# Optimization experiments

Measured on AMD Instinct MI355X. Metric: run time of the kernel, lower is better.

## Reference

```python
import jax, jax.numpy as jnp
import numpy as np

NEG = -9e15
ALPHA = 0.2  # LeakyReLU slope


def xavier(key, shape, gain=1.414):
    fan_in, fan_out = shape[-2], shape[-1]
    bound = gain * np.sqrt(6.0 / (fan_in + fan_out))
    return jax.random.uniform(key, shape, jnp.float32, -bound, bound)


def setup_inputs() -> dict:
    key = jax.random.key(0)
    ks = jax.random.split(key, 8)
    N, D_IN, HID, OUT, H = 4096, 128, 64, 64, 4
    x = jax.random.normal(ks[0], (N, D_IN), jnp.float32)
    adj = jax.random.randint(ks[1], (N, N), 0, 2, jnp.int32)
    # layer 0: in=D_IN, out=HID, heads=H
    W0 = xavier(ks[2], (H, D_IN, HID))
    a0 = xavier(ks[3], (H, 2 * HID, 1))
    # layer 1: in=HID*H, out=HID, heads=H
    W1 = xavier(ks[4], (H, HID * H, HID))
    a1 = xavier(ks[5], (H, 2 * HID, 1))
    # layer 2: in=HID*H, out=OUT, heads=1
    W2 = xavier(ks[6], (1, HID * H, OUT))
    a2 = xavier(ks[7], (1, 2 * OUT, 1))
    return {"x": x, "adj": adj, "W0": W0, "a0": a0, "W1": W1, "a1": a1, "W2": W2, "a2": a2}


def gat_layer(x, adj_mask, W, a):
    # x: [N, D], W: [H, D, O], a: [H, 2O, 1]
    O = W.shape[-1]
    h = jnp.einsum('nd,hdo->hno', x, W)                      # [H, N, O]
    a_l, a_r = a[:, :O, 0], a[:, O:, 0]                      # [H, O] each
    e_l = jnp.einsum('hno,ho->hn', h, a_l)                   # a^T[Wh_i||Wh_j] split
    e_r = jnp.einsum('hno,ho->hn', h, a_r)
    e = e_l[:, :, None] + e_r[:, None, :]                    # [H, N, N]
    e = jnp.where(e > 0, e, ALPHA * e)                       # LeakyReLU
    att = jnp.where(adj_mask[None], e, NEG)
    att = jax.nn.softmax(att, axis=-1)                       # dropout skipped (eval)
    out = jnp.einsum('hnm,hmo->hno', att, h)                 # [H, N, O]
    N = x.shape[0]
    return out.transpose(1, 0, 2).reshape(N, -1)             # [N, H*O]


def reference(x, adj, W0, a0, W1, a1, W2, a2):
    adj_mask = adj > 0
    h = gat_layer(x, adj_mask, W0, a0)
    h = jax.nn.elu(h)
    h = gat_layer(h, adj_mask, W1, a1)
    h = jax.nn.elu(h)
    h = gat_layer(h, adj_mask, W2, a2)
    return h
```

## Files before the change

### kernel.cpp

```cpp
#include <hip/hip_runtime.h>

#define LOG2E 1.4426950408889634f

typedef float  f32x4 __attribute__((ext_vector_type(4)));
typedef int    i32x4 __attribute__((ext_vector_type(4)));
typedef short  s16x8 __attribute__((ext_vector_type(8)));
typedef unsigned long long u64x2 __attribute__((ext_vector_type(2)));

static __device__ __forceinline__ float exp2_fast(float x) {
#if __has_builtin(__builtin_amdgcn_exp2f)
    return __builtin_amdgcn_exp2f(x);
#else
    return exp2f(x);
#endif
}
static __device__ __forceinline__ unsigned short bf16_rne(float f) {
    unsigned u = __float_as_uint(f);
    u += 0x7FFFu + ((u >> 16) & 1u);
    return (unsigned short)(u >> 16);
}
static __device__ __forceinline__ int sbfe1(unsigned w, int pos) {
#if __has_builtin(__builtin_amdgcn_sbfe)
    return __builtin_amdgcn_sbfe((int)w, pos, 1);
#else
    return (int)(w << (31 - pos)) >> 31;
#endif
}
static __device__ __forceinline__ unsigned pack_hi16(unsigned u1, unsigned u0) {
#if __has_builtin(__builtin_amdgcn_perm)
    return __builtin_amdgcn_perm(u1, u0, 0x07060302u);
#else
    return (u0 >> 16) | (u1 & 0xFFFF0000u);
#endif
}

__global__ __launch_bounds__(256) void prep_all(
    const float* __restrict__ xf, const int* __restrict__ adj,
    const float* __restrict__ W0, const float* __restrict__ W1,
    const float* __restrict__ W2,
    unsigned short* __restrict__ xc, unsigned long long* __restrict__ bits,
    unsigned short* __restrict__ W0t, unsigned short* __restrict__ W1t,
    unsigned short* __restrict__ W2t, unsigned* __restrict__ MxU)
{
    const int b = blockIdx.x, tid = threadIdx.x;
    if (b < 16384) {
        const int w = tid >> 6, lane = tid & 63;
        const int base = b * 1024 + w * 256;
        unsigned long long m[4];
#pragma unroll
        for (int r = 0; r < 4; ++r)
            m[r] = __ballot(adj[base + r * 64 + lane] != 0);
        if (lane == 0) {
            u64x2 lo = {m[0], m[1]}, hi = {m[2], m[3]};
            *(u64x2*)(bits + (base >> 6))     = lo;
            *(u64x2*)(bits + (base >> 6) + 2) = hi;
        }
    } else if (b < 18432) {
        int i = (b - 16384) * 256 + tid;
        xc[i] = bf16_rne(xf[i]);
    } else {
        int gid = (b - 18432) * 256 + tid;
        if (gid < 32768) {
            int h = gid >> 13, d = (gid >> 6) & 127, o = gid & 63;
            W0t[(h * 64 + o) * 128 + d] = bf16_rne(W0[gid]);
        } else if (gid < 98304) {
            int g = gid - 32768;
            int h = g >> 14, d = (g >> 6) & 255, o = g & 63;
            W1t[(h * 64 + o) * 256 + d] = bf16_rne(W1[g]);
        } else if (gid < 114688) {
            int g = gid - 98304;
            int d = g >> 6, o = g & 63;
            W2t[o * 256 + d] = bf16_rne(W2[g]);
        } else if (gid < 114700) {
            MxU[gid - 114688] = 0x007FFFFFu;
        }
    }
}

__global__ __launch_bounds__(256) void gemm_elr(
    const unsigned short* __restrict__ X, int K,
    const unsigned short* __restrict__ Wt,
    const float* __restrict__ a,
    unsigned short* __restrict__ hT,
    float* __restrict__ el2, float* __restrict__ er2,
    unsigned* __restrict__ MxU)
{
    const int lane = threadIdx.x & 63, w = threadIdx.x >> 6;
    const int c = lane & 15, q = lane >> 4;
    const int h = blockIdx.y;
    const int nb = blockIdx.x * 64 + w * 16;
    const unsigned short* xrow = X + (size_t)(nb + c) * K + q * 8;
    const unsigned short* wb   = Wt + ((size_t)h * 64 + c) * K + q * 8;

    f32x4 acc[4] = {{0,0,0,0},{0,0,0,0},{0,0,0,0},{0,0,0,0}};
    for (int kk = 0; kk < K; kk += 32) {
        s16x8 af = *(const s16x8*)(xrow + kk);
#pragma unroll
        for (int j = 0; j < 4; ++j) {
            s16x8 bf = *(const s16x8*)(wb + (size_t)(j * 16) * K + kk);
            acc[j] = __builtin_amdgcn_mfma_f32_16x16x32_bf16(af, bf, acc[j], 0, 0, 0);
        }
    }
#pragma unroll
    for (int j = 0; j < 4; ++j) {
        unsigned d0 = (unsigned)bf16_rne(acc[j][0]) | ((unsigned)bf16_rne(acc[j][1]) << 16);
        unsigned d1 = (unsigned)bf16_rne(acc[j][2]) | ((unsigned)bf16_rne(acc[j][3]) << 16);
        unsigned short* dst = hT + ((size_t)h * 64 + j * 16 + c) * 4096 + nb + q * 4;
        ((unsigned*)dst)[0] = d0;
        ((unsigned*)dst)[1] = d1;
    }
    const float* ab = a + h * 128;
    float elr[4] = {0,0,0,0}, err[4] = {0,0,0,0};
#pragma unroll
    for (int j = 0; j < 4; ++j) {
        float al = ab[j * 16 + c];
        float ar = ab[64 + j * 16 + c];
#pragma unroll
        for (int r = 0; r < 4; ++r) {
            elr[r] = fmaf(al, acc[j][r], elr[r]);
            err[r] = fmaf(ar, acc[j][r], err[r]);
        }
    }
#pragma unroll
    for (int m = 1; m <= 8; m <<= 1) {
#pragma unroll
        for (int r = 0; r < 4; ++r) {
            elr[r] += __shfl_xor(elr[r], m, 64);
            err[r] += __shfl_xor(err[r], m, 64);
        }
    }
    if (c == 0) {
#pragma unroll
        for (int r = 0; r < 4; ++r) {
            int n = nb + q * 4 + r;
            el2[h * 4096 + n] = elr[r] * LOG2E;
            er2[h * 4096 + n] = err[r] * LOG2E;
        }
    }
    float mm = fmaxf(fmaxf(err[0], err[1]), fmaxf(err[2], err[3]));
    mm = fmaxf(mm, __shfl_xor(mm, 16, 64));
    mm = fmaxf(mm, __shfl_xor(mm, 32, 64));
    if (lane == 0) {
        unsigned u = __float_as_uint(mm * LOG2E);
        unsigned key = (u & 0x80000000u) ? ~u : (u | 0x80000000u);
        atomicMax(MxU + h, key);
    }
}

__global__ __launch_bounds__(256) void att_kernel(
    const unsigned short* __restrict__ hT,
    const float* __restrict__ el2g, const float* __restrict__ er2g,
    const unsigned* __restrict__ MxU,
    const unsigned long long* __restrict__ bits,
    float* __restrict__ accP, float* __restrict__ lP,
    int H, int KPS, int HO)
{
    __shared__ unsigned short ldsH[64 * 256];
    __shared__ float ldsE[512];
    const int tid = threadIdx.x;
    const int lane = tid & 63, w = tid >> 6;
    const int c = lane & 15, q = lane >> 4, q8 = q * 8;
    const int h = blockIdx.y, ks = blockIdx.z;
    const int nb = blockIdx.x * 64 + w * 16;
    const int rowA = nb + c;

    unsigned kM = MxU[h];
    float M2 = __uint_as_float((kM & 0x80000000u) ? (kM & 0x7FFFFFFFu) : ~kM);
    float e2 = el2g[h * 4096 + rowA];
    float xx = e2 + M2;
    float C2 = fmaxf(xx, 0.2f * xx);
    const float Al = exp2_fast(xx - C2);
    const float Bl = exp2_fast(fmaf(0.2f, xx, -C2));

    const char* bitrow = (const char*)bits + (size_t)rowA * 512 + (size_t)(KPS >> 3) * ks;

    s16x8 ones = {0,0,0,0,0,0,0,0};
    if (c == 0) {
#pragma unroll
        for (int i = 0; i < 8; ++i) ones[i] = (short)0x3F80;
    }
    f32x4 acc[4] = {{0,0,0,0},{0,0,0,0},{0,0,0,0},{0,0,0,0}};
    f32x4 accl = {0,0,0,0};

    const unsigned short* hTh = hT + (size_t)h * 64 * 4096;
    const float* erh = er2g + h * 4096;
    const int tiles = KPS >> 8;

    for (int t = 0; t < tiles; ++t) {
        const int mabs = ks * KPS + t * 256;
#pragma unroll
        for (int i = 0; i < 8; ++i) {
            int cidx = i * 256 + tid;
            int o = cidx >> 5, seg = cidx & 31;
            i32x4 v = *(const i32x4*)(hTh + (size_t)o * 4096 + mabs + seg * 8);
            *(i32x4*)(ldsH + o * 256 + ((seg ^ (o & 7)) << 3)) = v;
        }
        {
            float er = erh[mabs + tid] - M2;
            ldsE[2 * tid]     = exp2_fast(er);
            ldsE[2 * tid + 1] = exp2_fast(0.2f * er);
        }
        __syncthreads();

        i32x4 b0 = *(const i32x4*)(bitrow + t * 32);
        i32x4 b1 = *(const i32x4*)(bitrow + t * 32 + 16);
        int bw[8] = {b0[0], b0[1], b0[2], b0[3], b1[0], b1[1], b1[2], b1[3]};

#pragma unroll
        for (int cc = 0; cc < 8; ++cc) {
            const int kl = cc * 32 + q8;
            const f32x4* ep = (const f32x4*)(ldsE + 2 * kl);
            f32x4 ev0 = ep[0], ev1 = ep[1], ev2 = ep[2], ev3 = ep[3];
            const unsigned word = (unsigned)bw[cc];
            unsigned pd[4];
#pragma unroll
            for (int jj = 0; jj < 4; ++jj) {
                f32x4 ev = (jj == 0) ? ev0 : (jj == 1) ? ev1 : (jj == 2) ? ev2 : ev3;
                float p0 = fmaxf(Al * ev[0], Bl * ev[1]);
                float p1 = fmaxf(Al * ev[2], Bl * ev[3]);
                unsigned u0 = __float_as_uint(p0) & (unsigned)sbfe1(word, q8 + 2 * jj);
                unsigned u1 = __float_as_uint(p1) & (unsigned)sbfe1(word, q8 + 2 * jj + 1);
                pd[jj] = pack_hi16(u1, u0);
            }
            union { unsigned u[4]; s16x8 s; } afu;
            afu.u[0] = pd[0]; afu.u[1] = pd[1]; afu.u[2] = pd[2]; afu.u[3] = pd[3];
            s16x8 af = afu.s;
            const int klx = kl ^ ((c & 7) << 3);
            const unsigned short* lb = ldsH + c * 256 + klx;
#pragma unroll
            for (int j = 0; j < 4; ++j) {
                s16x8 bf = *(const s16x8*)(lb + (size_t)(j * 16) * 256);
                acc[j] = __builtin_amdgcn_mfma_f32_16x16x32_bf16(af, bf, acc[j], 0, 0, 0);
            }
            accl = __builtin_amdgcn_mfma_f32_16x16x32_bf16(af, ones, accl, 0, 0, 0);
        }
        __syncthreads();
    }
    float ls[4];
#pragma unroll
    for (int r = 0; r < 4; ++r) ls[r] = __shfl(accl[r], lane & 48, 64);

    float* ap = accP + ((size_t)ks * 4096 + nb + q * 4) * HO + h * 64 + c;
#pragma unroll
    for (int r = 0; r < 4; ++r)
#pragma unroll
        for (int j = 0; j < 4; ++j)
            ap[(size_t)r * HO + j * 16] = acc[j][r];
    if (c == 0) {
#pragma unroll
        for (int r = 0; r < 4; ++r)
            lP[((size_t)ks * H + h) * 4096 + nb + q * 4 + r] = ls[r];
    }
}

__global__ __launch_bounds__(256) void comb_kernel(
    const float* __restrict__ accP, const float* __restrict__ lP,
    unsigned short* __restrict__ outb, float* __restrict__ outf,
    int KS, int H, int lgHO, int do_elu)
{
    const int idx = blockIdx.x * 256 + threadIdx.x;
    const int HO = 1 << lgHO;
    const int n = idx >> lgHO, col = idx & (HO - 1), h = col >> 6;
    float s = 0.f, l = 0.f;
    for (int ks = 0; ks < KS; ++ks) {
        s += accP[((size_t)ks * 4096 + n) * HO + col];
        l += lP[((size_t)ks * H + h) * 4096 + n];
    }
    float v = s / l;
    if (do_elu && v < 0.f) v = exp2_fast(v * LOG2E) - 1.f;
    if (outf) outf[idx] = v;
    else      outb[idx] = bf16_rne(v);
}

extern "C" void kernel_launch(void* const* d_in, const int* in_sizes, int n_in,
                              void* d_out, int out_size, void* d_ws, size_t ws_size,
                              hipStream_t stream)
{
    (void)in_sizes; (void)n_in; (void)out_size; (void)ws_size;
    const float* x   = (const float*)d_in[0];
    const int*   adj = (const int*)d_in[1];
    const float* W0  = (const float*)d_in[2];
    const float* a0  = (const float*)d_in[3];
    const float* W1  = (const float*)d_in[4];
    const float* a1  = (const float*)d_in[5];
    const float* W2  = (const float*)d_in[6];
    const float* a2  = (const float*)d_in[7];

    char* p = (char*)d_ws;
    unsigned long long* bits = (unsigned long long*)(p + 0x000000);
    unsigned short* hT  = (unsigned short*)(p + 0x200000);
    unsigned short* X12 = (unsigned short*)(p + 0x400000);
    unsigned short* Xc  = (unsigned short*)(p + 0x600000);
    unsigned short* W0t = (unsigned short*)(p + 0x700000);
    unsigned short* W1t = (unsigned short*)(p + 0x710000);
    unsigned short* W2t = (unsigned short*)(p + 0x730000);
    float*    el2  = (float*)(p + 0x738000);
    float*    er2  = (float*)(p + 0x748000);
    unsigned* MxU  = (unsigned*)(p + 0x758000);
    float*    accP = (float*)(p + 0x760000);
    float*    lP   = (float*)(p + 0xF60000);

    prep_all<<<18881, 256, 0, stream>>>(x, adj, W0, W1, W2, Xc, bits,
                                        W0t, W1t, W2t, MxU);

    gemm_elr<<<dim3(64, 4), 256, 0, stream>>>(Xc, 128, W0t, a0, hT, el2, er2, MxU + 0);
    att_kernel<<<dim3(64, 4, 2), 256, 0, stream>>>(hT, el2, er2, MxU + 0, bits, accP, lP, 4, 2048, 256);
    comb_kernel<<<4096, 256, 0, stream>>>(accP, lP, X12, nullptr, 2, 4, 8, 1);

    gemm_elr<<<dim3(64, 4), 256, 0, stream>>>(X12, 256, W1t, a1, hT, el2, er2, MxU + 4);
    att_kernel<<<dim3(64, 4, 2), 256, 0, stream>>>(hT, el2, er2, MxU + 4, bits, accP, lP, 4, 2048, 256);
    comb_kernel<<<4096, 256, 0, stream>>>(accP, lP, X12, nullptr, 2, 4, 8, 1);

    gemm_elr<<<dim3(64, 1), 256, 0, stream>>>(X12, 256, W2t, a2, hT, el2, er2, MxU + 8);
    att_kernel<<<dim3(64, 1, 4), 256, 0, stream>>>(hT, el2, er2, MxU + 8, bits, accP, lP, 1, 1024, 64);
    comb_kernel<<<1024, 256, 0, stream>>>(accP, lP, nullptr, (float*)d_out, 4, 1, 6, 0);
}
```

Measured before the change: 276.6 us.

## Double-buffer attention tiles with direct global-to-LDS loads and prefetch

```diff
diff --git a/kernel.cpp b/kernel.cpp
--- a/kernel.cpp
+++ b/kernel.cpp
@@ -155,8 +155,8 @@
     float* __restrict__ accP, float* __restrict__ lP,
     int H, int KPS, int HO)
 {
-    __shared__ unsigned short ldsH[64 * 256];
-    __shared__ float ldsE[512];
+    __shared__ unsigned short ldsH[2][64 * 256];
+    __shared__ float ldsE[2][512];
     const int tid = threadIdx.x;
     const int lane = tid & 63, w = tid >> 6;
     const int c = lane & 15, q = lane >> 4, q8 = q * 8;
@@ -173,44 +173,72 @@
     const float Bl = exp2_fast(fmaf(0.2f, xx, -C2));
 
     const char* bitrow = (const char*)bits + (size_t)rowA * 512 + (size_t)(KPS >> 3) * ks;
-
-    s16x8 ones = {0,0,0,0,0,0,0,0};
-    if (c == 0) {
-#pragma unroll
-        for (int i = 0; i < 8; ++i) ones[i] = (short)0x3F80;
-    }
-    f32x4 acc[4] = {{0,0,0,0},{0,0,0,0},{0,0,0,0},{0,0,0,0}};
-    f32x4 accl = {0,0,0,0};
-
     const unsigned short* hTh = hT + (size_t)h * 64 * 4096;
     const float* erh = er2g + h * 4096;
     const int tiles = KPS >> 8;
-
-    for (int t = 0; t < tiles; ++t) {
-        const int mabs = ks * KPS + t * 256;
+    const int kbase = ks * KPS;
+
+    auto STAGE = [&](int buf, int mabs_) {
 #pragma unroll
         for (int i = 0; i < 8; ++i) {
             int cidx = i * 256 + tid;
-            int o = cidx >> 5, seg = cidx & 31;
-            i32x4 v = *(const i32x4*)(hTh + (size_t)o * 4096 + mabs + seg * 8);
-            *(i32x4*)(ldsH + o * 256 + ((seg ^ (o & 7)) << 3)) = v;
-        }
-        {
-            float er = erh[mabs + tid] - M2;
-            ldsE[2 * tid]     = exp2_fast(er);
-            ldsE[2 * tid + 1] = exp2_fast(0.2f * er);
-        }
-        __syncthreads();
-
-        i32x4 b0 = *(const i32x4*)(bitrow + t * 32);
-        i32x4 b1 = *(const i32x4*)(bitrow + t * 32 + 16);
-        int bw[8] = {b0[0], b0[1], b0[2], b0[3], b1[0], b1[1], b1[2], b1[3]};
+            int o = cidx >> 5, g = cidx & 31;
+            const unsigned short* sp =
+                hTh + (size_t)o * 4096 + mabs_ + ((g ^ (o & 7)) << 3);
+            unsigned short* dp = &ldsH[buf][(i * 256 + (tid & ~63)) << 3];
+            __builtin_amdgcn_global_load_lds(
+                (const __attribute__((address_space(1))) void*)sp,
+                (__attribute__((address_space(3))) void*)dp, 16, 0, 0);
+        }
+    };
+
+    s16x8 ones = {0,0,0,0,0,0,0,0};
+    if (c == 0) {
+#pragma unroll
+        for (int i = 0; i < 8; ++i) ones[i] = (short)0x3F80;
+    }
+    f32x4 acc[4] = {{0,0,0,0},{0,0,0,0},{0,0,0,0},{0,0,0,0}};
+    f32x4 accl = {0,0,0,0};
+
+    STAGE(0, kbase);
+    {
+        float ee = erh[kbase + tid] - M2;
+        ldsE[0][2 * tid]     = exp2_fast(ee);
+        ldsE[0][2 * tid + 1] = exp2_fast(0.2f * ee);
+    }
+    i32x4 bA = *(const i32x4*)(bitrow);
+    i32x4 bB = *(const i32x4*)(bitrow + 16);
+    __syncthreads();
+
+    for (int t = 0; t < tiles; ++t) {
+        const int cur = t & 1, nxt = cur ^ 1;
+        const bool more = (t + 1 < tiles);
+        const unsigned short* Hc = ldsH[cur];
+        const float* Ec = ldsE[cur];
+
+        const f32x4* ep0 = (const f32x4*)(Ec + 2 * q8);
+        f32x4 nv0 = ep0[0], nv1 = ep0[1], nv2 = ep0[2], nv3 = ep0[3];
+
+        float ern = 0.f;
+        if (more) {
+            const int mn = kbase + (t + 1) * 256;
+            STAGE(nxt, mn);
+            ern = erh[mn + tid];
+        }
+        int bw[8] = {bA[0], bA[1], bA[2], bA[3], bB[0], bB[1], bB[2], bB[3]};
+        if (more) {
+            bA = *(const i32x4*)(bitrow + (t + 1) * 32);
+            bB = *(const i32x4*)(bitrow + (t + 1) * 32 + 16);
+        }
 
 #pragma unroll
         for (int cc = 0; cc < 8; ++cc) {
+            f32x4 ev0 = nv0, ev1 = nv1, ev2 = nv2, ev3 = nv3;
+            if (cc < 7) {
+                const f32x4* epn = (const f32x4*)(Ec + 2 * ((cc + 1) * 32 + q8));
+                nv0 = epn[0]; nv1 = epn[1]; nv2 = epn[2]; nv3 = epn[3];
+            }
             const int kl = cc * 32 + q8;
-            const f32x4* ep = (const f32x4*)(ldsE + 2 * kl);
-            f32x4 ev0 = ep[0], ev1 = ep[1], ev2 = ep[2], ev3 = ep[3];
             const unsigned word = (unsigned)bw[cc];
             unsigned pd[4];
 #pragma unroll
@@ -226,16 +254,25 @@
             afu.u[0] = pd[0]; afu.u[1] = pd[1]; afu.u[2] = pd[2]; afu.u[3] = pd[3];
             s16x8 af = afu.s;
             const int klx = kl ^ ((c & 7) << 3);
-            const unsigned short* lb = ldsH + c * 256 + klx;
+            const unsigned short* lb = Hc + c * 256 + klx;
+            __builtin_amdgcn_s_setprio(1);
 #pragma unroll
             for (int j = 0; j < 4; ++j) {
                 s16x8 bf = *(const s16x8*)(lb + (size_t)(j * 16) * 256);
                 acc[j] = __builtin_amdgcn_mfma_f32_16x16x32_bf16(af, bf, acc[j], 0, 0, 0);
             }
             accl = __builtin_amdgcn_mfma_f32_16x16x32_bf16(af, ones, accl, 0, 0, 0);
+            __builtin_amdgcn_s_setprio(0);
+        }
+
+        if (more) {
+            float ee = ern - M2;
+            ldsE[nxt][2 * tid]     = exp2_fast(ee);
+            ldsE[nxt][2 * tid + 1] = exp2_fast(0.2f * ee);
         }
         __syncthreads();
     }
+
     float ls[4];
 #pragma unroll
     for (int r = 0; r < 4; ++r) ls[r] = __shfl(accl[r], lane & 48, 64);
@@ -312,6 +349,6 @@
     comb_kernel<<<4096, 256, 0, stream>>>(accP, lP, X12, nullptr, 2, 4, 8, 1);
 
     gemm_elr<<<dim3(64, 1), 256, 0, stream>>>(X12, 256, W2t, a2, hT, el2, er2, MxU + 8);
-    att_kernel<<<dim3(64, 1, 4), 256, 0, stream>>>(hT, el2, er2, MxU + 8, bits, accP, lP, 1, 1024, 64);
-    comb_kernel<<<1024, 256, 0, stream>>>(accP, lP, nullptr, (float*)d_out, 4, 1, 6, 0);
-}
+    att_kernel<<<dim3(64, 1, 8), 256, 0, stream>>>(hT, el2, er2, MxU + 8, bits, accP, lP, 1, 512, 64);
+    comb_kernel<<<1024, 256, 0, stream>>>(accP, lP, nullptr, (float*)d_out, 8, 1, 6, 0);
+}
```

New measurement: 226.1 us. 18.3% less time.
